# Performance work log

Hardware: AMD Instinct MI355X
Metric: run time of the kernel (lower is better)

Reference implementation:

```python
import jax, jax.numpy as jnp
import numpy as np

B, N, D, H = 2, 1024, 1024, 16
DH = D // H
SCALE = 1.0 / DH ** 0.5
STJ_Q = 1.0
NUM_ITER = 4
CAUSAL = True
EPS = 1e-6


def setup_inputs() -> dict:
    key = jax.random.key(0)
    k1, k2, k3 = jax.random.split(key, 3)
    x = jax.random.normal(k1, (B, N, D), jnp.float32)
    Wqkv = jax.random.normal(k2, (3 * D, D), jnp.float32) / np.float32(np.sqrt(D))
    Wo = jax.random.normal(k3, (D, D), jnp.float32) / np.float32(np.sqrt(D))
    return {"x": x, "Wqkv": Wqkv, "Wo": Wo}


def stieltjes_attention(Q, K, V, scale, causal, q, num_iter):
    # Q,K,V: [B,H,N,dh]. Scores s: [B,H,N,N].
    n = Q.shape[2]
    s = jnp.einsum('bhnd,bhmd->bhnm', Q, K) * scale
    if causal:
        mask = jnp.tril(jnp.ones((n, n), bool))  # [N,N], True = attend
    else:
        mask = jnp.ones((n, n), bool)
    # Solve per-row lambda s.t. sum_j (lambda - s_j)^(-q) = 1 (Stieltjes-transform
    # normalization) with Newton iterations; masked entries contribute 0.
    s_masked = jnp.where(mask, s, -1e30)
    lam = s_masked.max(-1) + 1.0  # [B,H,N], start above max score
    for _ in range(num_iter):
        d = jnp.maximum(lam[..., None] - s, EPS)  # [B,H,N,N]
        w = jnp.where(mask, d ** (-q), 0.0)
        f = w.sum(-1) - 1.0
        fp = -q * jnp.where(mask, d ** (-q - 1.0), 0.0).sum(-1)
        lam = lam - f / fp
    d = jnp.maximum(lam[..., None] - s, EPS)
    p = jnp.where(mask, d ** (-q), 0.0)
    p = p / p.sum(-1, keepdims=True)  # final exact normalization
    return jnp.einsum('bhnm,bhmd->bhnd', p, V)


def reference(x, Wqkv, Wo):
    b, n, dmodel = x.shape
    qkv = (x @ Wqkv.T).reshape(b, n, 3, H, DH).transpose(2, 0, 3, 1, 4)
    Q, K, V = qkv[0], qkv[1], qkv[2]
    o = stieltjes_attention(Q, K, V, SCALE, CAUSAL, STJ_Q, NUM_ITER)
    o = o.transpose(0, 2, 1, 3).reshape(b, n, dmodel)
    return o @ Wo.T
```

## Files before the change

kernel.cpp:

```cpp
#include <hip/hip_runtime.h>
#include <hip/hip_bf16.h>
#include <math.h>

#define HNUM 16
#define DH 64
#define NSEQ 1024
#define BATCH 2
#define DMODEL 1024
#define SCALE 0.125f
#define EPS 1e-6f
#define NUM_ITER 4
#define SPAD_T 1080

typedef float f32x4 __attribute__((ext_vector_type(4)));
typedef short bfrag __attribute__((ext_vector_type(8)));
typedef unsigned int u32x4 __attribute__((ext_vector_type(4)));

__device__ inline float bf2f_u(unsigned int u) {
    return __builtin_bit_cast(float, u << 16);
}
__device__ inline unsigned short f2bf_u(float f) {
    return __builtin_bit_cast(unsigned short, __float2bfloat16(f));
}

__device__ inline void gload16(const __hip_bfloat16* g, __hip_bfloat16* l) {
    __builtin_amdgcn_global_load_lds(
        (const __attribute__((address_space(1))) void*)g,
        (__attribute__((address_space(3))) void*)l, 16, 0, 0);
}

__global__ __launch_bounds__(256) void cast3(const float* __restrict__ s0, __hip_bfloat16* __restrict__ d0, int n0,
                                             const float* __restrict__ s1, __hip_bfloat16* __restrict__ d1, int n1,
                                             const float* __restrict__ s2, __hip_bfloat16* __restrict__ d2, int n2) {
    const int stride = gridDim.x * blockDim.x;
    const int tot = n0 + n1 + n2;
    for (int i = blockIdx.x * blockDim.x + threadIdx.x; i < tot; i += stride) {
        const float* s; __hip_bfloat16* d; int off;
        if (i < n0)            { s = s0; d = d0; off = i; }
        else if (i < n0 + n1)  { s = s1; d = d1; off = i - n0; }
        else                   { s = s2; d = d2; off = i - n0 - n1; }
        const float4 v = *reinterpret_cast<const float4*>(&s[(size_t)off * 4]);
        ushort4 o;
        o.x = f2bf_u(v.x); o.y = f2bf_u(v.y); o.z = f2bf_u(v.z); o.w = f2bf_u(v.w);
        *reinterpret_cast<ushort4*>(&d[(size_t)off * 4]) = o;
    }
}

template <bool OUT_BF16>
__global__ __launch_bounds__(256) void gemm_bt(const __hip_bfloat16* __restrict__ A,
                                               const __hip_bfloat16* __restrict__ B,
                                               void* __restrict__ Cv,
                                               int M, int Nc, int K) {
    __shared__ __align__(16) __hip_bfloat16 As[64 * 64];
    __shared__ __align__(16) __hip_bfloat16 Bs[128 * 64];
    const int tid  = threadIdx.x;
    const int l    = tid & 63;
    const int wave = tid >> 6;
    const int m0 = blockIdx.y * 64, n0 = blockIdx.x * 128;
    const int wr = (wave >> 1) * 32, wc = (wave & 1) * 64;
    const int lr = l & 15;
    const int lk = (l >> 4) * 8;

    f32x4 acc[2][4];
#pragma unroll
    for (int m = 0; m < 2; ++m)
#pragma unroll
        for (int n = 0; n < 4; ++n) acc[m][n] = (f32x4){0.f, 0.f, 0.f, 0.f};

    for (int k0 = 0; k0 < K; k0 += 64) {
#pragma unroll
        for (int p = 0; p < 2; ++p) {
            const int idx = tid + p * 256;
            const int r = idx >> 3, ce = (idx & 7) * 8;
            gload16(&A[(size_t)(m0 + r) * K + k0 + ce], &As[idx * 8]);
        }
#pragma unroll
        for (int p = 0; p < 4; ++p) {
            const int idx = tid + p * 256;
            const int r = idx >> 3, ce = (idx & 7) * 8;
            gload16(&B[(size_t)(n0 + r) * K + k0 + ce], &Bs[idx * 8]);
        }
        __syncthreads();

#pragma unroll
        for (int kk = 0; kk < 64; kk += 32) {
            bfrag af[2], bfr[4];
#pragma unroll
            for (int m = 0; m < 2; ++m)
                af[m] = *reinterpret_cast<const bfrag*>(&As[(wr + m * 16 + lr) * 64 + kk + lk]);
#pragma unroll
            for (int n = 0; n < 4; ++n)
                bfr[n] = *reinterpret_cast<const bfrag*>(&Bs[(wc + n * 16 + lr) * 64 + kk + lk]);
#pragma unroll
            for (int m = 0; m < 2; ++m)
#pragma unroll
                for (int n = 0; n < 4; ++n)
                    acc[m][n] = __builtin_amdgcn_mfma_f32_16x16x32_bf16(
                        af[m], bfr[n], acc[m][n], 0, 0, 0);
        }
        __syncthreads();
    }

#pragma unroll
    for (int m = 0; m < 2; ++m) {
        const int row0 = m0 + wr + m * 16 + (l >> 4) * 4;
#pragma unroll
        for (int n = 0; n < 4; ++n) {
            const int col = n0 + wc + n * 16 + lr;
#pragma unroll
            for (int j = 0; j < 4; ++j) {
                if constexpr (OUT_BF16) {
                    ((__hip_bfloat16*)Cv)[(size_t)(row0 + j) * Nc + col] =
                        __float2bfloat16(acc[m][n][j]);
                } else {
                    ((float*)Cv)[(size_t)(row0 + j) * Nc + col] = acc[m][n][j];
                }
            }
        }
    }
}

__global__ __launch_bounds__(256) void transpose_v(const __hip_bfloat16* __restrict__ qkvb,
                                                   __hip_bfloat16* __restrict__ Vt) {
    const int bh = blockIdx.x >> 4;
    const int nc = blockIdx.x & 15;
    const int b = bh >> 4, h = bh & 15;
    __shared__ unsigned short tile[64][80];
    const int t = threadIdx.x;
    {
        const int r = t >> 2, cc = (t & 3) * 16;
        const size_t src = ((size_t)(b * NSEQ + nc * 64 + r)) * 3072 + 2048 + h * 64 + cc;
        const uint4 v0 = *reinterpret_cast<const uint4*>(&qkvb[src]);
        const uint4 v1 = *reinterpret_cast<const uint4*>(&qkvb[src + 8]);
        *reinterpret_cast<uint4*>(&tile[r][cc])     = v0;
        *reinterpret_cast<uint4*>(&tile[r][cc + 8]) = v1;
    }
    __syncthreads();
    {
        const int d = t >> 2, n2 = (t & 3) * 16;
        unsigned int e[16];
#pragma unroll
        for (int k = 0; k < 16; ++k) e[k] = tile[n2 + k][d];
        uint4 o0, o1;
        o0.x = e[0]  | (e[1]  << 16); o0.y = e[2]  | (e[3]  << 16);
        o0.z = e[4]  | (e[5]  << 16); o0.w = e[6]  | (e[7]  << 16);
        o1.x = e[8]  | (e[9]  << 16); o1.y = e[10] | (e[11] << 16);
        o1.z = e[12] | (e[13] << 16); o1.w = e[14] | (e[15] << 16);
        const size_t dst = ((size_t)(bh * 64 + d)) * 1024 + nc * 64 + n2;
        *reinterpret_cast<uint4*>(&Vt[dst])     = o0;
        *reinterpret_cast<uint4*>(&Vt[dst + 8]) = o1;
    }
}

template <int NQA, int NQB>
__device__ inline void newton2_wb(unsigned short* __restrict__ SA,
                                  unsigned short* __restrict__ SB,
                                  int ncolsA, int ncolsB,
                                  int limitA, int limitB, int lane) {
    constexpr int NCA = NQA * 2, NCB = NQB * 2;
    float svA[NCA * 2], svB[NCB * 2];
#pragma unroll
    for (int t = 0; t < NCA; ++t) {
        const int c = lane * 2 + t * 128;
        int ca = c;
        if (t >= NCA - 2) ca = (c < ncolsA) ? c : 0;
        const unsigned int u = *reinterpret_cast<const unsigned int*>(&SA[ca]);
        float v0 = bf2f_u(u & 0xffffu), v1 = bf2f_u(u >> 16);
        if (t >= NCA - 2) {
            v0 = (c     < ncolsA) ? v0 : -1e30f;
            v1 = (c + 1 < ncolsA) ? v1 : -1e30f;
        }
        svA[2 * t] = v0; svA[2 * t + 1] = v1;
    }
#pragma unroll
    for (int t = 0; t < NCB; ++t) {
        const int c = lane * 2 + t * 128;
        int cbm = c;
        if (t >= NCB - 2) cbm = (c < ncolsB) ? c : 0;
        const unsigned int u = *reinterpret_cast<const unsigned int*>(&SB[cbm]);
        float v0 = bf2f_u(u & 0xffffu), v1 = bf2f_u(u >> 16);
        if (t >= NCB - 2) {
            v0 = (c     < ncolsB) ? v0 : -1e30f;
            v1 = (c + 1 < ncolsB) ? v1 : -1e30f;
        }
        svB[2 * t] = v0; svB[2 * t + 1] = v1;
    }

    float mA = svA[0], mB = svB[0];
#pragma unroll
    for (int e = 1; e < 2 * NCA; ++e) mA = fmaxf(mA, svA[e]);
#pragma unroll
    for (int e = 1; e < 2 * NCB; ++e) mB = fmaxf(mB, svB[e]);
#pragma unroll
    for (int off = 32; off; off >>= 1) {
        mA = fmaxf(mA, __shfl_xor(mA, off));
        mB = fmaxf(mB, __shfl_xor(mB, off));
    }
    float lamA = mA + 1.0f, lamB = mB + 1.0f;

    for (int it = 0; it < NUM_ITER; ++it) {
        float fA = 0.f, fpA = 0.f, fB = 0.f, fpB = 0.f;
#pragma unroll
        for (int e = 0; e < 2 * NCA; ++e) {
            const float iA = __builtin_amdgcn_rcpf(fmaxf(lamA - svA[e], EPS));
            fA += iA; fpA = fmaf(iA, iA, fpA);
        }
#pragma unroll
        for (int e = 0; e < 2 * NCB; ++e) {
            const float iB = __builtin_amdgcn_rcpf(fmaxf(lamB - svB[e], EPS));
            fB += iB; fpB = fmaf(iB, iB, fpB);
        }
#pragma unroll
        for (int off = 32; off; off >>= 1) {
            fA += __shfl_xor(fA, off); fpA += __shfl_xor(fpA, off);
            fB += __shfl_xor(fB, off); fpB += __shfl_xor(fpB, off);
        }
        lamA += (fA - 1.0f) / fpA;
        lamB += (fB - 1.0f) / fpB;
    }

    float swA = 0.f, swB = 0.f;
#pragma unroll
    for (int e = 0; e < 2 * NCA; ++e) {
        svA[e] = __builtin_amdgcn_rcpf(fmaxf(lamA - svA[e], EPS)); swA += svA[e];
    }
#pragma unroll
    for (int e = 0; e < 2 * NCB; ++e) {
        svB[e] = __builtin_amdgcn_rcpf(fmaxf(lamB - svB[e], EPS)); swB += svB[e];
    }
#pragma unroll
    for (int off = 32; off; off >>= 1) {
        swA += __shfl_xor(swA, off);
        swB += __shfl_xor(swB, off);
    }
    const float iswA = __builtin_amdgcn_rcpf(swA);
    const float iswB = __builtin_amdgcn_rcpf(swB);

#pragma unroll
    for (int t = 0; t < NCA; ++t) {
        const int c = lane * 2 + t * 128;
        if (t * 128 < limitA && c < limitA) {
            const unsigned int pk = (unsigned)f2bf_u(svA[2 * t] * iswA)
                                  | ((unsigned)f2bf_u(svA[2 * t + 1] * iswA) << 16);
            *reinterpret_cast<unsigned int*>(&SA[c]) = pk;
        }
    }
#pragma unroll
    for (int t = 0; t < NCB; ++t) {
        const int c = lane * 2 + t * 128;
        if (t * 128 < limitB && c < limitB) {
            const unsigned int pk = (unsigned)f2bf_u(svB[2 * t] * iswB)
                                  | ((unsigned)f2bf_u(svB[2 * t + 1] * iswB) << 16);
            *reinterpret_cast<unsigned int*>(&SB[c]) = pk;
        }
    }
}

__global__ __launch_bounds__(512) void attn_mfma(const __hip_bfloat16* __restrict__ qkvb,
                                                 const __hip_bfloat16* __restrict__ Vt,
                                                 __hip_bfloat16* __restrict__ obf) {
    const int tid  = threadIdx.x;
    const int lane = tid & 63;
    const int wave = tid >> 6;
    const int pair = blockIdx.x & 31;
    const int bh = blockIdx.x >> 5;
    const int b = bh >> 4, h = bh & 15;
    const int qtA = pair, qtB = 63 - pair;
    const int r0A = qtA * 16, r0B = qtB * 16;
    const int sbBase = r0A + 32;

    __shared__ __align__(16) unsigned short S[16][SPAD_T];

    const size_t qbase = (size_t)(b * NSEQ) * 3072;
    const int lr  = lane & 15;
    const int lk8 = (lane >> 4) * 8;
    const int rj0 = (lane >> 4) * 4;

    const __hip_bfloat16* qrowA = qkvb + qbase + (size_t)(r0A + lr) * 3072 + h * 64;
    const __hip_bfloat16* qrowB = qkvb + qbase + (size_t)(r0B + lr) * 3072 + h * 64;
    const bfrag aA0 = *reinterpret_cast<const bfrag*>(&qrowA[lk8]);
    const bfrag aA1 = *reinterpret_cast<const bfrag*>(&qrowA[32 + lk8]);
    const bfrag aB0 = *reinterpret_cast<const bfrag*>(&qrowB[lk8]);
    const bfrag aB1 = *reinterpret_cast<const bfrag*>(&qrowB[32 + lk8]);
    const __hip_bfloat16* kglob = qkvb + qbase + 1024 + h * 64;

    const int ntA = qtA + 2, ntB = qtB + 2;
    for (int t = wave; t < ntA + ntB; t += 8) {
        const bool isA = (t < ntA);
        const int jt  = isA ? t : (t - ntA);
        const int qtX = isA ? qtA : qtB;
        const int cb  = isA ? 0 : sbBase;
        if (jt <= qtX) {
            const int jrow = jt * 16 + lr;
            const bfrag b0 = *reinterpret_cast<const bfrag*>(&kglob[(size_t)jrow * 3072 + lk8]);
            const bfrag b1 = *reinterpret_cast<const bfrag*>(&kglob[(size_t)jrow * 3072 + 32 + lk8]);
            f32x4 c = (f32x4){0.f, 0.f, 0.f, 0.f};
            c = __builtin_amdgcn_mfma_f32_16x16x32_bf16(isA ? aA0 : aB0, b0, c, 0, 0, 0);
            c = __builtin_amdgcn_mfma_f32_16x16x32_bf16(isA ? aA1 : aB1, b1, c, 0, 0, 0);
#pragma unroll
            for (int j = 0; j < 4; ++j)
                S[rj0 + j][cb + jt * 16 + lr] = f2bf_u(c[j] * SCALE);
        } else {
#pragma unroll
            for (int j = 0; j < 4; ++j)
                S[rj0 + j][cb + jt * 16 + lr] = 0;
        }
    }
    __syncthreads();

    {
        const int limitA = r0A + 16, limitB = r0B + 16;
        for (int p = 0; p < 2; ++p) {
            const int row = wave * 2 + p;
            const int ncolsA = r0A + row + 1, ncolsB = r0B + row + 1;
            if (qtA < 16)
                newton2_wb<1, 4>(&S[row][0], &S[row][sbBase],
                                 ncolsA, ncolsB, limitA, limitB, lane);
            else
                newton2_wb<2, 3>(&S[row][0], &S[row][sbBase],
                                 ncolsA, ncolsB, limitA, limitB, lane);
        }
    }
    __syncthreads();

    {
        const int tile = wave >> 2, dt = wave & 3;
        const int r0t = tile ? r0B : r0A;
        const int cb  = tile ? sbBase : 0;
        const __hip_bfloat16* vtrow = Vt + ((size_t)(bh * 64 + dt * 16 + lr)) * 1024;

        f32x4 acc0 = (f32x4){0.f, 0.f, 0.f, 0.f};
        f32x4 acc1 = (f32x4){0.f, 0.f, 0.f, 0.f};
        for (int j0 = 0; j0 <= r0t; j0 += 64) {
            {
                const bfrag pa = *reinterpret_cast<const bfrag*>(&S[lr][cb + j0 + lk8]);
                const bfrag pb = *reinterpret_cast<const bfrag*>(&vtrow[j0 + lk8]);
                acc0 = __builtin_amdgcn_mfma_f32_16x16x32_bf16(pa, pb, acc0, 0, 0, 0);
            }
            if (j0 + 32 <= r0t) {
                const bfrag pa = *reinterpret_cast<const bfrag*>(&S[lr][cb + j0 + 32 + lk8]);
                const bfrag pb = *reinterpret_cast<const bfrag*>(&vtrow[j0 + 32 + lk8]);
                acc1 = __builtin_amdgcn_mfma_f32_16x16x32_bf16(pa, pb, acc1, 0, 0, 0);
            }
        }

#pragma unroll
        for (int j = 0; j < 4; ++j) {
            const int row = rj0 + j;
            obf[(size_t)(b * NSEQ + r0t + row) * 1024 + h * 64 + dt * 16 + lr] =
                __float2bfloat16(acc0[j] + acc1[j]);
        }
    }
}

extern "C" void kernel_launch(void* const* d_in, const int* in_sizes, int n_in,
                              void* d_out, int out_size, void* d_ws, size_t ws_size,
                              hipStream_t stream) {
    const float* x    = (const float*)d_in[0];
    const float* Wqkv = (const float*)d_in[1];
    const float* Wo   = (const float*)d_in[2];
    float* out = (float*)d_out;

    const int M = BATCH * NSEQ;
    char* ws = (char*)d_ws;
    __hip_bfloat16* xbf  = (__hip_bfloat16*)ws; ws += (size_t)M * DMODEL * 2;
    __hip_bfloat16* wqbf = (__hip_bfloat16*)ws; ws += (size_t)3 * DMODEL * DMODEL * 2;
    __hip_bfloat16* wobf = (__hip_bfloat16*)ws; ws += (size_t)DMODEL * DMODEL * 2;
    __hip_bfloat16* qkvb = (__hip_bfloat16*)ws; ws += (size_t)M * 3 * DMODEL * 2;
    __hip_bfloat16* Vt   = (__hip_bfloat16*)ws; ws += (size_t)BATCH * HNUM * DH * NSEQ * 2;
    __hip_bfloat16* obf  = (__hip_bfloat16*)ws; ws += (size_t)M * DMODEL * 2;

    dim3 blk(256);
    cast3<<<2048, blk, 0, stream>>>(x, xbf, M * DMODEL / 4,
                                    Wqkv, wqbf, 3 * DMODEL * DMODEL / 4,
                                    Wo, wobf, DMODEL * DMODEL / 4);

    dim3 g1(3 * DMODEL / 128, M / 64);
    gemm_bt<true><<<g1, blk, 0, stream>>>(xbf, wqbf, qkvb, M, 3 * DMODEL, DMODEL);

    transpose_v<<<512, blk, 0, stream>>>(qkvb, Vt);

    attn_mfma<<<1024, dim3(512), 0, stream>>>(qkvb, Vt, obf);

    dim3 g2(DMODEL / 128, M / 64);
    gemm_bt<false><<<g2, blk, 0, stream>>>(obf, wobf, out, M, DMODEL, DMODEL);
}
```

Before: 115.4 us.

## Pack two 8-row query tiles per 16-row MFMA and shrink attention blocks

The attention kernel now processes two 8-row causal query tiles (front and back) in one 16-row MFMA, with 256-thread blocks and twice as many blocks. This balances causal work more finely and raises block-level parallelism. The per-row Newton template is chosen from the actual column counts, and the Newton division becomes a reciprocal multiply. The output projection moves to a new 64x64-tile GEMM to put more blocks on the CUs. The cost is more masking and branching logic in the score and PV stages, plus extra padding of the shared-memory score rows.

Result: slower. 129.2 us (+11.9%).

```diff
diff --git a/kernel.cpp b/kernel.cpp
--- a/kernel.cpp
+++ b/kernel.cpp
@@ -10,7 +10,7 @@
 #define SCALE 0.125f
 #define EPS 1e-6f
 #define NUM_ITER 4
-#define SPAD_T 1080
+#define SPAD_T 1096
 
 typedef float f32x4 __attribute__((ext_vector_type(4)));
 typedef short bfrag __attribute__((ext_vector_type(8)));
@@ -120,6 +120,73 @@
     }
 }
 
+__global__ __launch_bounds__(256) void gemm_bt64(const __hip_bfloat16* __restrict__ A,
+                                                 const __hip_bfloat16* __restrict__ B,
+                                                 float* __restrict__ C,
+                                                 int M, int Nc, int K) {
+    __shared__ __align__(16) __hip_bfloat16 As[64 * 64];
+    __shared__ __align__(16) __hip_bfloat16 Bs[64 * 64];
+    const int tid  = threadIdx.x;
+    const int l    = tid & 63;
+    const int wave = tid >> 6;
+    const int m0 = blockIdx.y * 64, n0 = blockIdx.x * 64;
+    const int wr = (wave >> 1) * 32, wc = (wave & 1) * 32;
+    const int lr = l & 15;
+    const int lk = (l >> 4) * 8;
+
+    f32x4 acc[2][2];
+#pragma unroll
+    for (int m = 0; m < 2; ++m)
+#pragma unroll
+        for (int n = 0; n < 2; ++n) acc[m][n] = (f32x4){0.f, 0.f, 0.f, 0.f};
+
+    for (int k0 = 0; k0 < K; k0 += 64) {
+#pragma unroll
+        for (int p = 0; p < 2; ++p) {
+            const int idx = tid + p * 256;
+            const int r = idx >> 3, ce = (idx & 7) * 8;
+            gload16(&A[(size_t)(m0 + r) * K + k0 + ce], &As[idx * 8]);
+        }
+#pragma unroll
+        for (int p = 0; p < 2; ++p) {
+            const int idx = tid + p * 256;
+            const int r = idx >> 3, ce = (idx & 7) * 8;
+            gload16(&B[(size_t)(n0 + r) * K + k0 + ce], &Bs[idx * 8]);
+        }
+        __syncthreads();
+
+#pragma unroll
+        for (int kk = 0; kk < 64; kk += 32) {
+            bfrag af[2], bfr[2];
+#pragma unroll
+            for (int m = 0; m < 2; ++m)
+                af[m] = *reinterpret_cast<const bfrag*>(&As[(wr + m * 16 + lr) * 64 + kk + lk]);
+#pragma unroll
+            for (int n = 0; n < 2; ++n)
+                bfr[n] = *reinterpret_cast<const bfrag*>(&Bs[(wc + n * 16 + lr) * 64 + kk + lk]);
+#pragma unroll
+            for (int m = 0; m < 2; ++m)
+#pragma unroll
+                for (int n = 0; n < 2; ++n)
+                    acc[m][n] = __builtin_amdgcn_mfma_f32_16x16x32_bf16(
+                        af[m], bfr[n], acc[m][n], 0, 0, 0);
+        }
+        __syncthreads();
+    }
+
+#pragma unroll
+    for (int m = 0; m < 2; ++m) {
+        const int row0 = m0 + wr + m * 16 + (l >> 4) * 4;
+#pragma unroll
+        for (int n = 0; n < 2; ++n) {
+            const int col = n0 + wc + n * 16 + lr;
+#pragma unroll
+            for (int j = 0; j < 4; ++j)
+                C[(size_t)(row0 + j) * Nc + col] = acc[m][n][j];
+        }
+    }
+}
+
 __global__ __launch_bounds__(256) void transpose_v(const __hip_bfloat16* __restrict__ qkvb,
                                                    __hip_bfloat16* __restrict__ Vt) {
     const int bh = blockIdx.x >> 4;
@@ -215,8 +282,8 @@
             fA += __shfl_xor(fA, off); fpA += __shfl_xor(fpA, off);
             fB += __shfl_xor(fB, off); fpB += __shfl_xor(fpB, off);
         }
-        lamA += (fA - 1.0f) / fpA;
-        lamB += (fB - 1.0f) / fpB;
+        lamA += (fA - 1.0f) * __builtin_amdgcn_rcpf(fpA);
+        lamB += (fB - 1.0f) * __builtin_amdgcn_rcpf(fpB);
     }
 
     float swA = 0.f, swB = 0.f;
@@ -256,98 +323,116 @@
     }
 }
 
-__global__ __launch_bounds__(512) void attn_mfma(const __hip_bfloat16* __restrict__ qkvb,
+__global__ __launch_bounds__(256) void attn_mfma(const __hip_bfloat16* __restrict__ qkvb,
                                                  const __hip_bfloat16* __restrict__ Vt,
                                                  __hip_bfloat16* __restrict__ obf) {
     const int tid  = threadIdx.x;
     const int lane = tid & 63;
     const int wave = tid >> 6;
-    const int pair = blockIdx.x & 31;
-    const int bh = blockIdx.x >> 5;
+    const int pair = blockIdx.x & 63;
+    const int bh = blockIdx.x >> 6;
     const int b = bh >> 4, h = bh & 15;
-    const int qtA = pair, qtB = 63 - pair;
-    const int r0A = qtA * 16, r0B = qtB * 16;
-    const int sbBase = r0A + 32;
-
-    __shared__ __align__(16) unsigned short S[16][SPAD_T];
+    const int qtA = pair, qtB = 127 - pair;
+    const int r0A = qtA * 8, r0B = qtB * 8;
+    const int W_A = (r0A + 8 + 63) & ~63;
+    const int W_B = (r0B + 8 + 63) & ~63;
+    const int limitA = (r0A + 8 + 15) & ~15;
+    const int limitB = (r0B + 8 + 15) & ~15;
+
+    __shared__ __align__(16) unsigned short S[8][SPAD_T];
 
     const size_t qbase = (size_t)(b * NSEQ) * 3072;
     const int lr  = lane & 15;
     const int lk8 = (lane >> 4) * 8;
     const int rj0 = (lane >> 4) * 4;
 
-    const __hip_bfloat16* qrowA = qkvb + qbase + (size_t)(r0A + lr) * 3072 + h * 64;
-    const __hip_bfloat16* qrowB = qkvb + qbase + (size_t)(r0B + lr) * 3072 + h * 64;
-    const bfrag aA0 = *reinterpret_cast<const bfrag*>(&qrowA[lk8]);
-    const bfrag aA1 = *reinterpret_cast<const bfrag*>(&qrowA[32 + lk8]);
-    const bfrag aB0 = *reinterpret_cast<const bfrag*>(&qrowB[lk8]);
-    const bfrag aB1 = *reinterpret_cast<const bfrag*>(&qrowB[32 + lk8]);
+    const int qabs = (lr < 8) ? (r0A + lr) : (r0B + (lr & 7));
+    const __hip_bfloat16* qrow = qkvb + qbase + (size_t)qabs * 3072 + h * 64;
+    const bfrag a0 = *reinterpret_cast<const bfrag*>(&qrow[lk8]);
+    const bfrag a1 = *reinterpret_cast<const bfrag*>(&qrow[32 + lk8]);
     const __hip_bfloat16* kglob = qkvb + qbase + 1024 + h * 64;
 
-    const int ntA = qtA + 2, ntB = qtB + 2;
-    for (int t = wave; t < ntA + ntB; t += 8) {
-        const bool isA = (t < ntA);
-        const int jt  = isA ? t : (t - ntA);
-        const int qtX = isA ? qtA : qtB;
-        const int cb  = isA ? 0 : sbBase;
-        if (jt <= qtX) {
-            const int jrow = jt * 16 + lr;
+    const int ntasks = W_B >> 4;
+    for (int jt = wave; jt < ntasks; jt += 4) {
+        const int col16 = jt << 4;
+        if (col16 < limitB) {
+            const int jrow = col16 + lr;
             const bfrag b0 = *reinterpret_cast<const bfrag*>(&kglob[(size_t)jrow * 3072 + lk8]);
             const bfrag b1 = *reinterpret_cast<const bfrag*>(&kglob[(size_t)jrow * 3072 + 32 + lk8]);
             f32x4 c = (f32x4){0.f, 0.f, 0.f, 0.f};
-            c = __builtin_amdgcn_mfma_f32_16x16x32_bf16(isA ? aA0 : aB0, b0, c, 0, 0, 0);
-            c = __builtin_amdgcn_mfma_f32_16x16x32_bf16(isA ? aA1 : aB1, b1, c, 0, 0, 0);
-#pragma unroll
-            for (int j = 0; j < 4; ++j)
-                S[rj0 + j][cb + jt * 16 + lr] = f2bf_u(c[j] * SCALE);
+            c = __builtin_amdgcn_mfma_f32_16x16x32_bf16(a0, b0, c, 0, 0, 0);
+            c = __builtin_amdgcn_mfma_f32_16x16x32_bf16(a1, b1, c, 0, 0, 0);
+#pragma unroll
+            for (int j = 0; j < 4; ++j) {
+                const int row = rj0 + j;
+                if (row < 8) {
+                    if (col16 < limitA)
+                        S[row][col16 + lr] = f2bf_u(c[j] * SCALE);
+                    else if (col16 < W_A)
+                        S[row][col16 + lr] = 0;
+                } else {
+                    S[row - 8][W_A + col16 + lr] = f2bf_u(c[j] * SCALE);
+                }
+            }
         } else {
 #pragma unroll
-            for (int j = 0; j < 4; ++j)
-                S[rj0 + j][cb + jt * 16 + lr] = 0;
+            for (int j = 0; j < 4; ++j) {
+                const int row = rj0 + j;
+                if (row >= 8) S[row - 8][W_A + col16 + lr] = 0;
+            }
         }
     }
     __syncthreads();
 
+    for (int p = 0; p < 2; ++p) {
+        const int row = wave * 2 + p;
+        const int ncolsA = r0A + row + 1;
+        const int ncolsB = r0B + row + 1;
+        const int key = ((ncolsA > 256) ? 2 : 0) | ((ncolsB > 768) ? 1 : 0);
+        switch (key) {
+            case 0:  newton2_wb<1, 3>(&S[row][0], &S[row][W_A], ncolsA, ncolsB, limitA, limitB, lane); break;
+            case 1:  newton2_wb<1, 4>(&S[row][0], &S[row][W_A], ncolsA, ncolsB, limitA, limitB, lane); break;
+            case 2:  newton2_wb<2, 3>(&S[row][0], &S[row][W_A], ncolsA, ncolsB, limitA, limitB, lane); break;
+            default: newton2_wb<2, 4>(&S[row][0], &S[row][W_A], ncolsA, ncolsB, limitA, limitB, lane); break;
+        }
+    }
+    __syncthreads();
+
     {
-        const int limitA = r0A + 16, limitB = r0B + 16;
-        for (int p = 0; p < 2; ++p) {
-            const int row = wave * 2 + p;
-            const int ncolsA = r0A + row + 1, ncolsB = r0B + row + 1;
-            if (qtA < 16)
-                newton2_wb<1, 4>(&S[row][0], &S[row][sbBase],
-                                 ncolsA, ncolsB, limitA, limitB, lane);
-            else
-                newton2_wb<2, 3>(&S[row][0], &S[row][sbBase],
-                                 ncolsA, ncolsB, limitA, limitB, lane);
-        }
-    }
-    __syncthreads();
-
-    {
-        const int tile = wave >> 2, dt = wave & 3;
-        const int r0t = tile ? r0B : r0A;
-        const int cb  = tile ? sbBase : 0;
+        const int dt = wave;
         const __hip_bfloat16* vtrow = Vt + ((size_t)(bh * 64 + dt * 16 + lr)) * 1024;
+        const int srow = lr & 7;
+        const unsigned int bmask = (lr < 8) ? 0u : 0xffffffffu;
 
         f32x4 acc0 = (f32x4){0.f, 0.f, 0.f, 0.f};
         f32x4 acc1 = (f32x4){0.f, 0.f, 0.f, 0.f};
-        for (int j0 = 0; j0 <= r0t; j0 += 64) {
-            {
-                const bfrag pa = *reinterpret_cast<const bfrag*>(&S[lr][cb + j0 + lk8]);
-                const bfrag pb = *reinterpret_cast<const bfrag*>(&vtrow[j0 + lk8]);
-                acc0 = __builtin_amdgcn_mfma_f32_16x16x32_bf16(pa, pb, acc0, 0, 0, 0);
-            }
-            if (j0 + 32 <= r0t) {
-                const bfrag pa = *reinterpret_cast<const bfrag*>(&S[lr][cb + j0 + 32 + lk8]);
-                const bfrag pb = *reinterpret_cast<const bfrag*>(&vtrow[j0 + 32 + lk8]);
-                acc1 = __builtin_amdgcn_mfma_f32_16x16x32_bf16(pa, pb, acc1, 0, 0, 0);
-            }
+        for (int j0 = 0; j0 < W_A; j0 += 64) {
+            const int scol = ((lr < 8) ? 0 : W_A) + j0 + lk8;
+            const bfrag pa0 = *reinterpret_cast<const bfrag*>(&S[srow][scol]);
+            const bfrag pa1 = *reinterpret_cast<const bfrag*>(&S[srow][scol + 32]);
+            const bfrag vb0 = *reinterpret_cast<const bfrag*>(&vtrow[j0 + lk8]);
+            const bfrag vb1 = *reinterpret_cast<const bfrag*>(&vtrow[j0 + 32 + lk8]);
+            acc0 = __builtin_amdgcn_mfma_f32_16x16x32_bf16(pa0, vb0, acc0, 0, 0, 0);
+            acc1 = __builtin_amdgcn_mfma_f32_16x16x32_bf16(pa1, vb1, acc1, 0, 0, 0);
+        }
+        for (int j0 = W_A; j0 < W_B; j0 += 64) {
+            u32x4 u0 = *reinterpret_cast<const u32x4*>(&S[srow][W_A + j0 + lk8]);
+            u32x4 u1 = *reinterpret_cast<const u32x4*>(&S[srow][W_A + j0 + 32 + lk8]);
+#pragma unroll
+            for (int k = 0; k < 4; ++k) { u0[k] &= bmask; u1[k] &= bmask; }
+            const bfrag pa0 = __builtin_bit_cast(bfrag, u0);
+            const bfrag pa1 = __builtin_bit_cast(bfrag, u1);
+            const bfrag vb0 = *reinterpret_cast<const bfrag*>(&vtrow[j0 + lk8]);
+            const bfrag vb1 = *reinterpret_cast<const bfrag*>(&vtrow[j0 + 32 + lk8]);
+            acc0 = __builtin_amdgcn_mfma_f32_16x16x32_bf16(pa0, vb0, acc0, 0, 0, 0);
+            acc1 = __builtin_amdgcn_mfma_f32_16x16x32_bf16(pa1, vb1, acc1, 0, 0, 0);
         }
 
 #pragma unroll
         for (int j = 0; j < 4; ++j) {
             const int row = rj0 + j;
-            obf[(size_t)(b * NSEQ + r0t + row) * 1024 + h * 64 + dt * 16 + lr] =
+            const int r_abs = (row < 8) ? (r0A + row) : (r0B + row - 8);
+            obf[(size_t)(b * NSEQ + r_abs) * 1024 + h * 64 + dt * 16 + lr] =
                 __float2bfloat16(acc0[j] + acc1[j]);
         }
     }
@@ -380,8 +465,8 @@
 
     transpose_v<<<512, blk, 0, stream>>>(qkvb, Vt);
 
-    attn_mfma<<<1024, dim3(512), 0, stream>>>(qkvb, Vt, obf);
-
-    dim3 g2(DMODEL / 128, M / 64);
-    gemm_bt<false><<<g2, blk, 0, stream>>>(obf, wobf, out, M, DMODEL, DMODEL);
-}
+    attn_mfma<<<2048, blk, 0, stream>>>(qkvb, Vt, obf);
+
+    dim3 g2(DMODEL / 64, M / 64);
+    gemm_bt64<<<g2, blk, 0, stream>>>(obf, wobf, out, M, DMODEL, DMODEL);
+}
```

## Fuse fp32-to-bf16 casts into GEMM tile loads and drop cast kernel

Applied to the files above, without the earlier changes.

Removes the standalone cast kernel by having both projection GEMMs load fp32 tiles of x/Wqkv/Wo directly, convert them to bf16 in registers, and store them into shared memory. This cuts one launch and the write-then-reread of bf16 copies of the weights and input. In exchange, the GEMMs read twice the bytes per tile and lose the async global-to-LDS load path, and activations/weights are re-converted by every block that loads them. The output GEMM also moves to 64x64 tiles for more blocks, and the Newton update's divide becomes a hardware reciprocal.

After: 129.8 us. 1.12x slower.

```diff
diff --git a/kernel.cpp b/kernel.cpp
--- a/kernel.cpp
+++ b/kernel.cpp
@@ -22,6 +22,11 @@
 __device__ inline unsigned short f2bf_u(float f) {
     return __builtin_bit_cast(unsigned short, __float2bfloat16(f));
 }
+__device__ inline ushort4 cvt4(const float4 v) {
+    ushort4 o;
+    o.x = f2bf_u(v.x); o.y = f2bf_u(v.y); o.z = f2bf_u(v.z); o.w = f2bf_u(v.w);
+    return o;
+}
 
 __device__ inline void gload16(const __hip_bfloat16* g, __hip_bfloat16* l) {
     __builtin_amdgcn_global_load_lds(
@@ -29,28 +34,10 @@
         (__attribute__((address_space(3))) void*)l, 16, 0, 0);
 }
 
-__global__ __launch_bounds__(256) void cast3(const float* __restrict__ s0, __hip_bfloat16* __restrict__ d0, int n0,
-                                             const float* __restrict__ s1, __hip_bfloat16* __restrict__ d1, int n1,
-                                             const float* __restrict__ s2, __hip_bfloat16* __restrict__ d2, int n2) {
-    const int stride = gridDim.x * blockDim.x;
-    const int tot = n0 + n1 + n2;
-    for (int i = blockIdx.x * blockDim.x + threadIdx.x; i < tot; i += stride) {
-        const float* s; __hip_bfloat16* d; int off;
-        if (i < n0)            { s = s0; d = d0; off = i; }
-        else if (i < n0 + n1)  { s = s1; d = d1; off = i - n0; }
-        else                   { s = s2; d = d2; off = i - n0 - n1; }
-        const float4 v = *reinterpret_cast<const float4*>(&s[(size_t)off * 4]);
-        ushort4 o;
-        o.x = f2bf_u(v.x); o.y = f2bf_u(v.y); o.z = f2bf_u(v.z); o.w = f2bf_u(v.w);
-        *reinterpret_cast<ushort4*>(&d[(size_t)off * 4]) = o;
-    }
-}
-
-template <bool OUT_BF16>
-__global__ __launch_bounds__(256) void gemm_bt(const __hip_bfloat16* __restrict__ A,
-                                               const __hip_bfloat16* __restrict__ B,
-                                               void* __restrict__ Cv,
-                                               int M, int Nc, int K) {
+__global__ __launch_bounds__(256) void gemm1_cvt(const float* __restrict__ A,
+                                                 const float* __restrict__ B,
+                                                 __hip_bfloat16* __restrict__ C,
+                                                 int M, int Nc, int K) {
     __shared__ __align__(16) __hip_bfloat16 As[64 * 64];
     __shared__ __align__(16) __hip_bfloat16 Bs[128 * 64];
     const int tid  = threadIdx.x;
@@ -68,17 +55,28 @@
         for (int n = 0; n < 4; ++n) acc[m][n] = (f32x4){0.f, 0.f, 0.f, 0.f};
 
     for (int k0 = 0; k0 < K; k0 += 64) {
-#pragma unroll
-        for (int p = 0; p < 2; ++p) {
-            const int idx = tid + p * 256;
-            const int r = idx >> 3, ce = (idx & 7) * 8;
-            gload16(&A[(size_t)(m0 + r) * K + k0 + ce], &As[idx * 8]);
-        }
+        float4 la[4], lb[8];
 #pragma unroll
         for (int p = 0; p < 4; ++p) {
             const int idx = tid + p * 256;
-            const int r = idx >> 3, ce = (idx & 7) * 8;
-            gload16(&B[(size_t)(n0 + r) * K + k0 + ce], &Bs[idx * 8]);
+            const int r = idx >> 4, c4 = (idx & 15) * 4;
+            la[p] = *reinterpret_cast<const float4*>(&A[(size_t)(m0 + r) * K + k0 + c4]);
+        }
+#pragma unroll
+        for (int p = 0; p < 8; ++p) {
+            const int idx = tid + p * 256;
+            const int r = idx >> 4, c4 = (idx & 15) * 4;
+            lb[p] = *reinterpret_cast<const float4*>(&B[(size_t)(n0 + r) * K + k0 + c4]);
+        }
+#pragma unroll
+        for (int p = 0; p < 4; ++p) {
+            const int idx = tid + p * 256;
+            *reinterpret_cast<ushort4*>(&As[(idx >> 4) * 64 + (idx & 15) * 4]) = cvt4(la[p]);
+        }
+#pragma unroll
+        for (int p = 0; p < 8; ++p) {
+            const int idx = tid + p * 256;
+            *reinterpret_cast<ushort4*>(&Bs[(idx >> 4) * 64 + (idx & 15) * 4]) = cvt4(lb[p]);
         }
         __syncthreads();
 
@@ -108,14 +106,81 @@
         for (int n = 0; n < 4; ++n) {
             const int col = n0 + wc + n * 16 + lr;
 #pragma unroll
-            for (int j = 0; j < 4; ++j) {
-                if constexpr (OUT_BF16) {
-                    ((__hip_bfloat16*)Cv)[(size_t)(row0 + j) * Nc + col] =
-                        __float2bfloat16(acc[m][n][j]);
-                } else {
-                    ((float*)Cv)[(size_t)(row0 + j) * Nc + col] = acc[m][n][j];
-                }
-            }
+            for (int j = 0; j < 4; ++j)
+                C[(size_t)(row0 + j) * Nc + col] = __float2bfloat16(acc[m][n][j]);
+        }
+    }
+}
+
+__global__ __launch_bounds__(256) void gemm2_cvt(const __hip_bfloat16* __restrict__ A,
+                                                 const float* __restrict__ B,
+                                                 float* __restrict__ C,
+                                                 int M, int Nc, int K) {
+    __shared__ __align__(16) __hip_bfloat16 As[64 * 64];
+    __shared__ __align__(16) __hip_bfloat16 Bs[64 * 64];
+    const int tid  = threadIdx.x;
+    const int l    = tid & 63;
+    const int wave = tid >> 6;
+    const int m0 = blockIdx.y * 64, n0 = blockIdx.x * 64;
+    const int wr = (wave >> 1) * 32, wc = (wave & 1) * 32;
+    const int lr = l & 15;
+    const int lk = (l >> 4) * 8;
+
+    f32x4 acc[2][2];
+#pragma unroll
+    for (int m = 0; m < 2; ++m)
+#pragma unroll
+        for (int n = 0; n < 2; ++n) acc[m][n] = (f32x4){0.f, 0.f, 0.f, 0.f};
+
+    for (int k0 = 0; k0 < K; k0 += 64) {
+#pragma unroll
+        for (int p = 0; p < 2; ++p) {
+            const int idx = tid + p * 256;
+            const int r = idx >> 3, ce = (idx & 7) * 8;
+            gload16(&A[(size_t)(m0 + r) * K + k0 + ce], &As[idx * 8]);
+        }
+        float4 lb[4];
+#pragma unroll
+        for (int p = 0; p < 4; ++p) {
+            const int idx = tid + p * 256;
+            const int r = idx >> 4, c4 = (idx & 15) * 4;
+            lb[p] = *reinterpret_cast<const float4*>(&B[(size_t)(n0 + r) * K + k0 + c4]);
+        }
+#pragma unroll
+        for (int p = 0; p < 4; ++p) {
+            const int idx = tid + p * 256;
+            *reinterpret_cast<ushort4*>(&Bs[(idx >> 4) * 64 + (idx & 15) * 4]) = cvt4(lb[p]);
+        }
+        __syncthreads();
+
+#pragma unroll
+        for (int kk = 0; kk < 64; kk += 32) {
+            bfrag af[2], bfr[2];
+#pragma unroll
+            for (int m = 0; m < 2; ++m)
+                af[m] = *reinterpret_cast<const bfrag*>(&As[(wr + m * 16 + lr) * 64 + kk + lk]);
+#pragma unroll
+            for (int n = 0; n < 2; ++n)
+                bfr[n] = *reinterpret_cast<const bfrag*>(&Bs[(wc + n * 16 + lr) * 64 + kk + lk]);
+#pragma unroll
+            for (int m = 0; m < 2; ++m)
+#pragma unroll
+                for (int n = 0; n < 2; ++n)
+                    acc[m][n] = __builtin_amdgcn_mfma_f32_16x16x32_bf16(
+                        af[m], bfr[n], acc[m][n], 0, 0, 0);
+        }
+        __syncthreads();
+    }
+
+#pragma unroll
+    for (int m = 0; m < 2; ++m) {
+        const int row0 = m0 + wr + m * 16 + (l >> 4) * 4;
+#pragma unroll
+        for (int n = 0; n < 2; ++n) {
+            const int col = n0 + wc + n * 16 + lr;
+#pragma unroll
+            for (int j = 0; j < 4; ++j)
+                C[(size_t)(row0 + j) * Nc + col] = acc[m][n][j];
         }
     }
 }
@@ -215,8 +280,8 @@
             fA += __shfl_xor(fA, off); fpA += __shfl_xor(fpA, off);
             fB += __shfl_xor(fB, off); fpB += __shfl_xor(fpB, off);
         }
-        lamA += (fA - 1.0f) / fpA;
-        lamB += (fB - 1.0f) / fpB;
+        lamA += (fA - 1.0f) * __builtin_amdgcn_rcpf(fpA);
+        lamB += (fB - 1.0f) * __builtin_amdgcn_rcpf(fpB);
     }
 
     float swA = 0.f, swB = 0.f;
@@ -363,25 +428,19 @@
 
     const int M = BATCH * NSEQ;
     char* ws = (char*)d_ws;
-    __hip_bfloat16* xbf  = (__hip_bfloat16*)ws; ws += (size_t)M * DMODEL * 2;
-    __hip_bfloat16* wqbf = (__hip_bfloat16*)ws; ws += (size_t)3 * DMODEL * DMODEL * 2;
-    __hip_bfloat16* wobf = (__hip_bfloat16*)ws; ws += (size_t)DMODEL * DMODEL * 2;
     __hip_bfloat16* qkvb = (__hip_bfloat16*)ws; ws += (size_t)M * 3 * DMODEL * 2;
     __hip_bfloat16* Vt   = (__hip_bfloat16*)ws; ws += (size_t)BATCH * HNUM * DH * NSEQ * 2;
     __hip_bfloat16* obf  = (__hip_bfloat16*)ws; ws += (size_t)M * DMODEL * 2;
 
     dim3 blk(256);
-    cast3<<<2048, blk, 0, stream>>>(x, xbf, M * DMODEL / 4,
-                                    Wqkv, wqbf, 3 * DMODEL * DMODEL / 4,
-                                    Wo, wobf, DMODEL * DMODEL / 4);
 
     dim3 g1(3 * DMODEL / 128, M / 64);
-    gemm_bt<true><<<g1, blk, 0, stream>>>(xbf, wqbf, qkvb, M, 3 * DMODEL, DMODEL);
+    gemm1_cvt<<<g1, blk, 0, stream>>>(x, Wqkv, qkvb, M, 3 * DMODEL, DMODEL);
 
     transpose_v<<<512, blk, 0, stream>>>(qkvb, Vt);
 
     attn_mfma<<<1024, dim3(512), 0, stream>>>(qkvb, Vt, obf);
 
-    dim3 g2(DMODEL / 128, M / 64);
-    gemm_bt<false><<<g2, blk, 0, stream>>>(obf, wobf, out, M, DMODEL, DMODEL);
-}
+    dim3 g2(DMODEL / 64, M / 64);
+    gemm2_cvt<<<g2, blk, 0, stream>>>(obf, Wo, out, M, DMODEL, DMODEL);
+}
```
